# Kernel tuning notes

Hardware: AMD Instinct MI355X
Metric: run time of the kernel (lower is better)

The kernel has to match this reference:

```python
import jax, jax.numpy as jnp
import numpy as np

HID = 128
NEG = 9000000000000000.0  # 9e15 additive mask constant from the source


def setup_inputs() -> dict:
    key = jax.random.key(0)
    ks = jax.random.split(key, 20)
    B, N, OBS, N1, N2 = 32, 2048, 256, 8, 8
    x = jax.random.normal(ks[0], (B, N, OBS), dtype=jnp.float32)
    mask = jax.random.randint(ks[1], (B, N, N), 0, 2).astype(jnp.float32)

    def lin(kw, kb, fan_in, fan_out):
        bound = 1.0 / np.sqrt(fan_in)
        W = jax.random.uniform(kw, (fan_in, fan_out), jnp.float32, -bound, bound)
        b = jax.random.uniform(kb, (fan_out,), jnp.float32, -bound, bound)
        return W, b

    Wv, bv = lin(ks[2], ks[3], OBS, HID)
    Wk, bk = lin(ks[4], ks[5], OBS, HID)
    Wq, bq = lin(ks[6], ks[7], OBS, HID)
    Wout, bout = lin(ks[8], ks[9], HID, HID)
    Wval, bval = lin(ks[10], ks[11], HID, 1)
    Wadv1, badv1 = lin(ks[12], ks[13], HID, N1)
    Wadv2, badv2 = lin(ks[14], ks[15], HID, N2)
    return {
        'x': x, 'mask': mask,
        'Wv': Wv, 'bv': bv, 'Wk': Wk, 'bk': bk, 'Wq': Wq, 'bq': bq,
        'Wout': Wout, 'bout': bout, 'Wval': Wval, 'bval': bval,
        'Wadv1': Wadv1, 'badv1': badv1, 'Wadv2': Wadv2, 'badv2': badv2,
    }


def reference(x, mask, Wv, bv, Wk, bk, Wq, bq, Wout, bout,
              Wval, bval, Wadv1, badv1, Wadv2, badv2):
    # AttenModel
    v = jax.nn.relu(x @ Wv + bv)          # [B,N,H]
    q = jax.nn.relu(x @ Wq + bq)          # [B,N,H]
    k = jax.nn.relu(x @ Wk + bk)          # [B,N,H]
    scores = jnp.einsum('bnh,bmh->bnm', q, k)          # [B,N,N]
    scores = scores * mask - NEG * (1.0 - mask)
    att = jax.nn.softmax(scores, axis=2)
    out = jnp.einsum('bnm,bmh->bnh', att, v)            # [B,N,H]
    out = jax.nn.relu(out @ Wout + bout)                # [B,N,H]
    # Dueling heads (batch > 1, so squeeze(0) is a no-op)
    value = out @ Wval + bval                            # [B,N,1]
    adv1 = out @ Wadv1 + badv1                           # [B,N,n1]
    adv2 = out @ Wadv2 + badv2                           # [B,N,n2]
    q1 = value + adv1 - adv1.mean(axis=1, keepdims=True)
    q2 = value + adv2 - adv2.mean(axis=1, keepdims=True)
    return (q1, q2)
```

## Files before the change

### kernel.cpp

```cpp
#include <hip/hip_runtime.h>
#include <hip/hip_bf16.h>


typedef __attribute__((ext_vector_type(4))) float f32x4;
typedef __attribute__((ext_vector_type(8))) short bf16x8;
typedef __attribute__((ext_vector_type(4))) unsigned int u32x4;

#define LOG2E 1.44269504088896340736f
#define NEGC 9.0e15f

static __device__ __forceinline__ unsigned short f2bf(float f) {
  unsigned int x = __builtin_bit_cast(unsigned int, f);
  unsigned int r = (x + 0x7fffu + ((x >> 16) & 1u)) >> 16;
  return (unsigned short)r;
}
static __device__ __forceinline__ float bf2f(unsigned short u) {
  return __builtin_bit_cast(float, ((unsigned int)u) << 16);
}
static __device__ __forceinline__ unsigned int pack2bf(float lo, float hi) {
  return (unsigned int)f2bf(lo) | ((unsigned int)f2bf(hi) << 16);
}
static __device__ __forceinline__ f32x4 mfma16(bf16x8 a, bf16x8 b, f32x4 c) {
  return __builtin_amdgcn_mfma_f32_16x16x32_bf16(a, b, c, 0, 0, 0);
}

__global__ __launch_bounds__(256) void prepack_kernel(const float* __restrict__ mask,
                                                      unsigned long long* __restrict__ bits) {
  const int lane = threadIdx.x & 63;
  const int gwave = (blockIdx.x << 2) | (threadIdx.x >> 6);
  for (int r = 0; r < 8; ++r) {
    const long row = (long)gwave * 8 + r;
    const float* mp = mask + row * 2048 + lane;
    unsigned long long* op = bits + row * 32;
#pragma unroll
    for (int g = 0; g < 8; ++g) {
      float f0 = mp[(g * 4 + 0) * 64];
      float f1 = mp[(g * 4 + 1) * 64];
      float f2 = mp[(g * 4 + 2) * 64];
      float f3 = mp[(g * 4 + 3) * 64];
      unsigned long long b0 = __ballot(f0 != 0.0f);
      unsigned long long b1 = __ballot(f1 != 0.0f);
      unsigned long long b2 = __ballot(f2 != 0.0f);
      unsigned long long b3 = __ballot(f3 != 0.0f);
      if (lane == 0) {
        ulonglong2 w0 = {b0, b1};
        ulonglong2 w1 = {b2, b3};
        *(ulonglong2*)(op + g * 4) = w0;
        *(ulonglong2*)(op + g * 4 + 2) = w1;
      }
    }
  }
}

__global__ __launch_bounds__(256) void prep_kernel(
    const float* __restrict__ Wv, const float* __restrict__ Wk,
    const float* __restrict__ Wq, const float* __restrict__ Wout,
    unsigned short* __restrict__ Wf_hi, unsigned short* __restrict__ Wf_lo,
    unsigned short* __restrict__ WoutT) {
  int gid = blockIdx.x * 256 + threadIdx.x;
  if (gid < 12288) {
    int kc = gid / 1536;
    int rem = gid - kc * 1536;
    int t = rem >> 6, lane = rem & 63;
    int hf = lane & 15, qf = lane >> 4;
    int sec = t >> 3;
    int j = (t & 7) * 16 + hf;
    const float* W = (sec == 0) ? Wq : (sec == 1) ? Wk : Wv;
#pragma unroll
    for (int e = 0; e < 8; ++e) {
      int k = kc * 32 + qf * 8 + e;
      float w = W[k * 128 + j];
      unsigned short hi = f2bf(w);
      Wf_hi[gid * 8 + e] = hi;
      Wf_lo[gid * 8 + e] = f2bf(w - bf2f(hi));
    }
  } else if (gid < 12288 + 16384) {
    int i2 = gid - 12288;
    int j = i2 >> 7, c = i2 & 127;
    WoutT[i2] = f2bf(Wout[c * 128 + j]);
  }
}

__global__ __launch_bounds__(512, 2) void proj_kernel(
    const float* __restrict__ x,
    const unsigned short* __restrict__ Wf_hi, const unsigned short* __restrict__ Wf_lo,
    const float* __restrict__ bq, const float* __restrict__ bk, const float* __restrict__ bv,
    unsigned short* __restrict__ q_bf, unsigned short* __restrict__ Kf,
    unsigned short* __restrict__ Vf) {
  __shared__ bf16x8 wst_hi[1536];
  __shared__ bf16x8 wst_lo[1536];
  __shared__ unsigned short vbuf[128][136];

  const int tid = threadIdx.x;
  const int lane = tid & 63, wid = tid >> 6;
  const int qq = lane >> 4, hh = lane & 15;
  const long rbase = (long)blockIdx.x * 128;
  const long rowA = rbase + wid * 16 + hh;
  const f32x4 zero4 = {0.f, 0.f, 0.f, 0.f};
  f32x4 acc[24];
#pragma unroll
  for (int t = 0; t < 24; ++t) acc[t] = zero4;

  for (int kc = 0; kc < 8; ++kc) {
    __syncthreads();
#pragma unroll
    for (int i = 0; i < 3; ++i) {
      int idx = i * 512 + tid;
      wst_hi[idx] = *(const bf16x8*)(Wf_hi + ((long)kc * 1536 + idx) * 8);
      wst_lo[idx] = *(const bf16x8*)(Wf_lo + ((long)kc * 1536 + idx) * 8);
    }
    __syncthreads();

    const float* xp = x + rowA * 256 + kc * 32 + qq * 8;
    f32x4 x0 = *(const f32x4*)xp;
    f32x4 x1 = *(const f32x4*)(xp + 4);
    bf16x8 ah, al;
#pragma unroll
    for (int j = 0; j < 8; ++j) {
      float f = (j < 4) ? x0[j] : x1[j - 4];
      unsigned short h = f2bf(f);
      ah[j] = (short)h;
      al[j] = (short)f2bf(f - bf2f(h));
    }
#pragma unroll
    for (int t = 0; t < 24; ++t) {
      bf16x8 bh = wst_hi[t * 64 + lane];
      bf16x8 bl = wst_lo[t * 64 + lane];
      acc[t] = mfma16(ah, bh, acc[t]);
      acc[t] = mfma16(al, bh, acc[t]);
      acc[t] = mfma16(ah, bl, acc[t]);
    }
  }

  const int rowL = wid * 16 + qq * 4;
  const int b = (int)(rbase >> 11);
  const int tbase = (int)((rbase & 2047) >> 6);

  for (int sec = 0; sec < 3; ++sec) {
    __syncthreads();
#pragma unroll
    for (int tp = 0; tp < 8; ++tp) {
      const int t = sec * 8 + tp;
      const int j = tp * 16 + hh;
      const float bias = (sec == 0) ? bq[j] : (sec == 1) ? bk[j] : bv[j];
#pragma unroll
      for (int r = 0; r < 4; ++r) {
        unsigned short h = f2bf(fmaxf(acc[t][r] + bias, 0.f));
        if (sec == 2) vbuf[j][rowL + r] = h;
        else          vbuf[rowL + r][j] = h;
      }
    }
    __syncthreads();
    if (sec == 0) {
      const int row = tid >> 2, ch = tid & 3;
      bf16x8 w = *(const bf16x8*)&vbuf[row][ch * 32];
      bf16x8 w2 = *(const bf16x8*)&vbuf[row][ch * 32 + 8];
      bf16x8 w3 = *(const bf16x8*)&vbuf[row][ch * 32 + 16];
      bf16x8 w4 = *(const bf16x8*)&vbuf[row][ch * 32 + 24];
      unsigned short* op = q_bf + (rbase + row) * 128 + ch * 32;
      *(bf16x8*)op = w; *(bf16x8*)(op + 8) = w2;
      *(bf16x8*)(op + 16) = w3; *(bf16x8*)(op + 24) = w4;
    } else if (sec == 1) {
#pragma unroll
      for (int it = 0; it < 4; ++it) {
        int gid = it * 512 + tid;
        int tt = gid >> 10, m = (gid >> 8) & 3, kc = (gid >> 6) & 3, ln = gid & 63;
        int hf = ln & 15, qf = ln >> 4;
        bf16x8 w = *(const bf16x8*)&vbuf[tt * 64 + m * 16 + hf][kc * 32 + qf * 8];
        long off = (((long)(b * 32 + tbase + tt) * 16 + m * 4 + kc) * 64 + ln) * 8;
        *(bf16x8*)(Kf + off) = w;
      }
    } else {
#pragma unroll
      for (int it = 0; it < 4; ++it) {
        int gid = it * 512 + tid;
        int tt = gid >> 10, ht = (gid >> 7) & 7, c = (gid >> 6) & 1, ln = gid & 63;
        int hf = ln & 15, qf = ln >> 4;
        bf16x8 w = *(const bf16x8*)&vbuf[ht * 16 + hf][tt * 64 + c * 32 + qf * 8];
        long off = (((long)(b * 32 + tbase + tt) * 16 + ht * 2 + c) * 64 + ln) * 8;
        *(bf16x8*)(Vf + off) = w;
      }
    }
  }
}

__global__ __launch_bounds__(512, 2) void attn_kernel(
    const unsigned short* __restrict__ q_bf, const unsigned short* __restrict__ Kf,
    const unsigned short* __restrict__ Vf,
    const unsigned long long* __restrict__ bits, unsigned short* __restrict__ out_att) {
  __shared__ bf16x8 kls[2][1024];
  __shared__ bf16x8 vls[2][1024];

  const int tid = threadIdx.x;
  const int lane = tid & 63, wid = tid >> 6;
  const int qq = lane >> 4, hh = lane & 15;
  const int orig = blockIdx.x;
  const int b = ((orig & 7) << 2) | ((orig >> 3) & 3);
  const int nb = orig >> 5;
  const long qbase = (long)b * 2048 + nb * 256 + wid * 32;

  const f32x4 zero4 = {0.f, 0.f, 0.f, 0.f};

  bf16x8 qh[2][4];
#pragma unroll
  for (int ctq = 0; ctq < 2; ++ctq)
#pragma unroll
    for (int kc = 0; kc < 4; ++kc)
      qh[ctq][kc] = *(const bf16x8*)(q_bf + (qbase + ctq * 16 + hh) * 128 + kc * 32 + qq * 8);

  const unsigned long long* br0 = bits + (qbase + hh) * 32;
  const unsigned long long* br1 = bits + (qbase + 16 + hh) * 32;
  const unsigned short* kf0 = Kf + (long)(b * 32) * 8192;
  const unsigned short* vf0 = Vf + (long)(b * 32) * 8192;

  f32x4 o_acc[8][2];
#pragma unroll
  for (int ht = 0; ht < 8; ++ht) { o_acc[ht][0] = zero4; o_acc[ht][1] = zero4; }
  float m_run[2] = {-3.0e38f, -3.0e38f};
  float l_run[2] = {0.f, 0.f};

  bf16x8 stg[4];
  const int seg0 = wid * 4;
  auto LOADREG = [&](int t) {
#pragma unroll
    for (int i = 0; i < 4; ++i) {
      int seg = seg0 + i;
      const unsigned short* src = (seg < 16)
          ? kf0 + (long)t * 8192 + (seg * 64 + lane) * 8
          : vf0 + (long)t * 8192 + ((seg - 16) * 64 + lane) * 8;
      stg[i] = *(const bf16x8*)src;
    }
  };
  auto WRITEBUF = [&](int nb2) {
#pragma unroll
    for (int i = 0; i < 4; ++i) {
      int seg = seg0 + i;
      if (seg < 16) kls[nb2][seg * 64 + lane] = stg[i];
      else          vls[nb2][(seg - 16) * 64 + lane] = stg[i];
    }
  };

  LOADREG(0);
  WRITEBUF(0);
  LOADREG(1);
  __syncthreads();

  unsigned long long bc0 = br0[0];
  unsigned long long bc1 = br1[0];

  const int src0 = (((qq << 1)) & 3) * 16 + hh;
  const int src1 = (((qq << 1) + 1) & 3) * 16 + hh;
  const bool hiq = qq >= 2;
  int cur = 0;

  for (int t = 0; t < 32; ++t) {
    unsigned long long bn0 = 0, bn1 = 0;
    if (t + 1 < 32) { bn0 = br0[t + 1]; bn1 = br1[t + 1]; }

    f32x4 s[2][4];
#pragma unroll
    for (int m = 0; m < 4; ++m) { s[0][m] = zero4; s[1][m] = zero4; }
#pragma unroll
    for (int m = 0; m < 4; ++m) {
      bf16x8 khf[4];
#pragma unroll
      for (int kc = 0; kc < 4; ++kc) khf[kc] = kls[cur][(m * 4 + kc) * 64 + lane];
#pragma unroll
      for (int kc = 0; kc < 4; ++kc)
#pragma unroll
        for (int ctq = 0; ctq < 2; ++ctq)
          s[ctq][m] = mfma16(khf[kc], qh[ctq][kc], s[ctq][m]);
    }

    {
      const unsigned long long bb0 = bc0 >> (qq * 4);
      const unsigned long long bb1 = bc1 >> (qq * 4);
#pragma unroll
      for (int m = 0; m < 4; ++m)
#pragma unroll
        for (int r = 0; r < 4; ++r) {
          const int sh = m * 16 + r;
          s[0][m][r] = ((bb0 >> sh) & 1ull) ? s[0][m][r] : -NEGC;
          s[1][m][r] = ((bb1 >> sh) & 1ull) ? s[1][m][r] : -NEGC;
        }
    }

    unsigned int pk[2][4][2];
#pragma unroll
    for (int ctq = 0; ctq < 2; ++ctq) {
      float mx = s[ctq][0][0];
#pragma unroll
      for (int m = 0; m < 4; ++m)
#pragma unroll
        for (int r = 0; r < 4; ++r) mx = fmaxf(mx, s[ctq][m][r]);
      mx = fmaxf(mx, __shfl_xor(mx, 16, 64));
      mx = fmaxf(mx, __shfl_xor(mx, 32, 64));
      if (__any(mx > m_run[ctq])) {
        float mnew = fmaxf(m_run[ctq], mx);
        float sc = exp2f((m_run[ctq] - mnew) * LOG2E);
        m_run[ctq] = mnew;
        l_run[ctq] *= sc;
#pragma unroll
        for (int ht = 0; ht < 8; ++ht) o_acc[ht][ctq] *= sc;
      }
      float ps = 0.f;
#pragma unroll
      for (int m = 0; m < 4; ++m)
#pragma unroll
        for (int r = 0; r < 4; ++r) {
          float p = exp2f((s[ctq][m][r] - m_run[ctq]) * LOG2E);
          s[ctq][m][r] = p;
          ps += p;
        }
      ps += __shfl_xor(ps, 16, 64);
      ps += __shfl_xor(ps, 32, 64);
      l_run[ctq] += ps;
#pragma unroll
      for (int m = 0; m < 4; ++m) {
        pk[ctq][m][0] = pack2bf(s[ctq][m][0], s[ctq][m][1]);
        pk[ctq][m][1] = pack2bf(s[ctq][m][2], s[ctq][m][3]);
      }
    }

    bf16x8 pb[2][2];
#pragma unroll
    for (int ctq = 0; ctq < 2; ++ctq)
#pragma unroll
      for (int c = 0; c < 2; ++c) {
        unsigned int a0 = (unsigned int)__shfl((int)pk[ctq][2 * c][0], src0, 64);
        unsigned int a1 = (unsigned int)__shfl((int)pk[ctq][2 * c][1], src0, 64);
        unsigned int a2 = (unsigned int)__shfl((int)pk[ctq][2 * c][0], src1, 64);
        unsigned int a3 = (unsigned int)__shfl((int)pk[ctq][2 * c][1], src1, 64);
        unsigned int b0 = (unsigned int)__shfl((int)pk[ctq][2 * c + 1][0], src0, 64);
        unsigned int b1 = (unsigned int)__shfl((int)pk[ctq][2 * c + 1][1], src0, 64);
        unsigned int b2 = (unsigned int)__shfl((int)pk[ctq][2 * c + 1][0], src1, 64);
        unsigned int b3 = (unsigned int)__shfl((int)pk[ctq][2 * c + 1][1], src1, 64);
        u32x4 w;
        w[0] = hiq ? b0 : a0;
        w[1] = hiq ? b1 : a1;
        w[2] = hiq ? b2 : a2;
        w[3] = hiq ? b3 : a3;
        pb[ctq][c] = __builtin_bit_cast(bf16x8, w);
      }

#pragma unroll
    for (int ht = 0; ht < 8; ++ht)
#pragma unroll
      for (int c = 0; c < 2; ++c) {
        bf16x8 vf = vls[cur][(ht * 2 + c) * 64 + lane];
#pragma unroll
        for (int ctq = 0; ctq < 2; ++ctq)
          o_acc[ht][ctq] = mfma16(vf, pb[ctq][c], o_acc[ht][ctq]);
      }

    __syncthreads();
    if (t + 1 < 32) WRITEBUF(cur ^ 1);
    if (t + 2 < 32) LOADREG(t + 2);
    __syncthreads();
    cur ^= 1;
    bc0 = bn0;
    bc1 = bn1;
  }

#pragma unroll
  for (int ctq = 0; ctq < 2; ++ctq) {
    float inv = 1.0f / l_run[ctq];
    const long row = qbase + ctq * 16 + hh;
#pragma unroll
    for (int ht = 0; ht < 8; ++ht) {
      f32x4 o = o_acc[ht][ctq];
      uint2 w;
      w.x = pack2bf(o[0] * inv, o[1] * inv);
      w.y = pack2bf(o[2] * inv, o[3] * inv);
      *(uint2*)(out_att + row * 128 + ht * 16 + qq * 4) = w;
    }
  }
}

__global__ __launch_bounds__(256) void wout_heads_kernel(
    const unsigned short* __restrict__ out_att, const unsigned short* __restrict__ WoutT,
    const float* __restrict__ bout,
    const float* __restrict__ Wval, const float* __restrict__ bval,
    const float* __restrict__ Wadv1, const float* __restrict__ badv1,
    const float* __restrict__ Wadv2, const float* __restrict__ badv2,
    float* __restrict__ value, float* __restrict__ adv1, float* __restrict__ adv2) {
  const int lane = threadIdx.x & 63, wid = threadIdx.x >> 6;
  const int qq = lane >> 4, hh = lane & 15;
  const long rowA = (long)blockIdx.x * 64 + wid * 16 + hh;
  const f32x4 zero4 = {0.f, 0.f, 0.f, 0.f};
  f32x4 acc[8];
#pragma unroll
  for (int t = 0; t < 8; ++t) acc[t] = zero4;
#pragma unroll
  for (int kc = 0; kc < 4; ++kc) {
    bf16x8 af = *(const bf16x8*)(out_att + rowA * 128 + kc * 32 + qq * 8);
#pragma unroll
    for (int t = 0; t < 8; ++t) {
      bf16x8 bf = *(const bf16x8*)(WoutT + (t * 16 + hh) * 128 + kc * 32 + qq * 8);
      acc[t] = mfma16(af, bf, acc[t]);
    }
  }
  float pv[4] = {0.f, 0.f, 0.f, 0.f};
  float pa1[4][8], pa2[4][8];
#pragma unroll
  for (int r = 0; r < 4; ++r)
#pragma unroll
    for (int j = 0; j < 8; ++j) { pa1[r][j] = 0.f; pa2[r][j] = 0.f; }
#pragma unroll
  for (int t = 0; t < 8; ++t) {
    const int col = t * 16 + hh;
    const float bo = bout[col];
    const float wv = Wval[col];
    const f32x4 w1a = *(const f32x4*)(Wadv1 + col * 8);
    const f32x4 w1b = *(const f32x4*)(Wadv1 + col * 8 + 4);
    const f32x4 w2a = *(const f32x4*)(Wadv2 + col * 8);
    const f32x4 w2b = *(const f32x4*)(Wadv2 + col * 8 + 4);
#pragma unroll
    for (int r = 0; r < 4; ++r) {
      float h = fmaxf(acc[t][r] + bo, 0.f);
      pv[r] += h * wv;
#pragma unroll
      for (int j = 0; j < 4; ++j) {
        pa1[r][j]     += h * w1a[j];
        pa1[r][4 + j] += h * w1b[j];
        pa2[r][j]     += h * w2a[j];
        pa2[r][4 + j] += h * w2b[j];
      }
    }
  }
#pragma unroll
  for (int r = 0; r < 4; ++r) {
#pragma unroll
    for (int s = 1; s < 16; s <<= 1) {
      pv[r] += __shfl_xor(pv[r], s, 64);
#pragma unroll
      for (int j = 0; j < 8; ++j) {
        pa1[r][j] += __shfl_xor(pa1[r][j], s, 64);
        pa2[r][j] += __shfl_xor(pa2[r][j], s, 64);
      }
    }
  }
  if (hh == 0) {
    const float bv0 = bval[0];
#pragma unroll
    for (int r = 0; r < 4; ++r) {
      const long row = (long)blockIdx.x * 64 + wid * 16 + qq * 4 + r;
      value[row] = pv[r] + bv0;
#pragma unroll
      for (int j = 0; j < 8; ++j) {
        adv1[row * 8 + j] = pa1[r][j] + badv1[j];
        adv2[row * 8 + j] = pa2[r][j] + badv2[j];
      }
    }
  }
}

__global__ __launch_bounds__(256) void sums_kernel(const float* __restrict__ adv1,
                                                   const float* __restrict__ adv2,
                                                   float* __restrict__ sums) {
  const int b = blockIdx.x, tid = threadIdx.x;
  __shared__ float red[4][16];
  float p[16];
#pragma unroll
  for (int j = 0; j < 16; ++j) p[j] = 0.f;
  for (int n = tid; n < 2048; n += 256) {
    const long row = (long)b * 2048 + n;
    const f32x4 a1a = *(const f32x4*)(adv1 + row * 8);
    const f32x4 a1b = *(const f32x4*)(adv1 + row * 8 + 4);
    const f32x4 a2a = *(const f32x4*)(adv2 + row * 8);
    const f32x4 a2b = *(const f32x4*)(adv2 + row * 8 + 4);
#pragma unroll
    for (int j = 0; j < 4; ++j) {
      p[j] += a1a[j]; p[4 + j] += a1b[j];
      p[8 + j] += a2a[j]; p[12 + j] += a2b[j];
    }
  }
#pragma unroll
  for (int s = 1; s < 64; s <<= 1)
#pragma unroll
    for (int j = 0; j < 16; ++j) p[j] += __shfl_xor(p[j], s, 64);
  const int wid = tid >> 6;
  if ((tid & 63) == 0)
#pragma unroll
    for (int j = 0; j < 16; ++j) red[wid][j] = p[j];
  __syncthreads();
  if (tid < 16)
    sums[b * 16 + tid] = red[0][tid] + red[1][tid] + red[2][tid] + red[3][tid];
}

__global__ void combine_kernel(const float* __restrict__ value, const float* __restrict__ adv1,
                               const float* __restrict__ adv2, const float* __restrict__ sums,
                               float* __restrict__ out) {
  const int idx = blockIdx.x * 256 + threadIdx.x;
  const int half = 524288;
  const int which = (idx >= half) ? 1 : 0;
  const int rem = idx - which * half;
  const int b = rem >> 14;
  const int r2 = rem & 16383;
  const int n = r2 >> 3, j = r2 & 7;
  const long row = (long)b * 2048 + n;
  const float* adv = which ? adv2 : adv1;
  const float mean = sums[b * 16 + which * 8 + j] * (1.0f / 2048.0f);
  out[idx] = value[row] + adv[row * 8 + j] - mean;
}

extern "C" void kernel_launch(void* const* d_in, const int* in_sizes, int n_in,
                              void* d_out, int out_size, void* d_ws, size_t ws_size,
                              hipStream_t stream) {
  const float* x     = (const float*)d_in[0];
  const float* mask  = (const float*)d_in[1];
  const float* Wv    = (const float*)d_in[2];
  const float* bv    = (const float*)d_in[3];
  const float* Wk    = (const float*)d_in[4];
  const float* bk    = (const float*)d_in[5];
  const float* Wq    = (const float*)d_in[6];
  const float* bq    = (const float*)d_in[7];
  const float* Wout  = (const float*)d_in[8];
  const float* bout  = (const float*)d_in[9];
  const float* Wval  = (const float*)d_in[10];
  const float* bval  = (const float*)d_in[11];
  const float* Wadv1 = (const float*)d_in[12];
  const float* badv1 = (const float*)d_in[13];
  const float* Wadv2 = (const float*)d_in[14];
  const float* badv2 = (const float*)d_in[15];
  float* out = (float*)d_out;
  char* ws = (char*)d_ws;

  unsigned short* q_bf   = (unsigned short*)(ws + 0);
  unsigned short* Kf     = (unsigned short*)(ws + 16777216);
  unsigned short* Vf     = (unsigned short*)(ws + 33554432);
  unsigned short* out_at = (unsigned short*)(ws + 50331648);
  float* value = (float*)(ws + 67108864);
  float* adv1  = (float*)(ws + 67371008);
  float* adv2  = (float*)(ws + 69468160);
  float* sums  = (float*)(ws + 71565312);
  unsigned short* Wf_hi = (unsigned short*)(ws + 71567360);
  unsigned short* Wf_lo = (unsigned short*)(ws + 71763968);
  unsigned short* WoutT = (unsigned short*)(ws + 71960576);
  unsigned long long* bits = (unsigned long long*)(ws + 71993344);

  prepack_kernel<<<2048, 256, 0, stream>>>(mask, bits);
  prep_kernel<<<112, 256, 0, stream>>>(Wv, Wk, Wq, Wout, Wf_hi, Wf_lo, WoutT);
  proj_kernel<<<512, 512, 0, stream>>>(x, Wf_hi, Wf_lo, bq, bk, bv, q_bf, Kf, Vf);
  attn_kernel<<<256, 512, 0, stream>>>(q_bf, Kf, Vf, bits, out_at);
  wout_heads_kernel<<<1024, 256, 0, stream>>>(out_at, WoutT, bout, Wval, bval,
                                              Wadv1, badv1, Wadv2, badv2,
                                              value, adv1, adv2);
  sums_kernel<<<32, 256, 0, stream>>>(adv1, adv2, sums);
  combine_kernel<<<4096, 256, 0, stream>>>(value, adv1, adv2, sums, out);
}
```

Baseline: 362.9 us.

## Overlap LDS buffer writes with MFMA compute, vectorize mask bit-packing

The attention loop now writes the next K/V tile into the alternate LDS buffer and issues the following global load at the start of each iteration, before the MFMA work. This drops one of the two barriers per iteration and lets stores overlap with compute. MFMA sections are wrapped in s_setprio to favour matrix issue across waves. The mask prepack kernel switches from per-element ballots to float4 loads plus nibble packing combined with xor shuffles, giving coalesced vector reads.

```diff
diff --git a/kernel.cpp b/kernel.cpp
--- a/kernel.cpp
+++ b/kernel.cpp
@@ -28,26 +28,22 @@
                                                       unsigned long long* __restrict__ bits) {
   const int lane = threadIdx.x & 63;
   const int gwave = (blockIdx.x << 2) | (threadIdx.x >> 6);
+  const int sub = lane & 15, grp = lane >> 4;
   for (int r = 0; r < 8; ++r) {
     const long row = (long)gwave * 8 + r;
-    const float* mp = mask + row * 2048 + lane;
+    const float* mp = mask + row * 2048;
     unsigned long long* op = bits + row * 32;
 #pragma unroll
     for (int g = 0; g < 8; ++g) {
-      float f0 = mp[(g * 4 + 0) * 64];
-      float f1 = mp[(g * 4 + 1) * 64];
-      float f2 = mp[(g * 4 + 2) * 64];
-      float f3 = mp[(g * 4 + 3) * 64];
-      unsigned long long b0 = __ballot(f0 != 0.0f);
-      unsigned long long b1 = __ballot(f1 != 0.0f);
-      unsigned long long b2 = __ballot(f2 != 0.0f);
-      unsigned long long b3 = __ballot(f3 != 0.0f);
-      if (lane == 0) {
-        ulonglong2 w0 = {b0, b1};
-        ulonglong2 w1 = {b2, b3};
-        *(ulonglong2*)(op + g * 4) = w0;
-        *(ulonglong2*)(op + g * 4 + 2) = w1;
-      }
+      f32x4 v = *(const f32x4*)(mp + g * 256 + lane * 4);
+      unsigned int nib = (v[0] != 0.f ? 1u : 0u) | (v[1] != 0.f ? 2u : 0u)
+                       | (v[2] != 0.f ? 4u : 0u) | (v[3] != 0.f ? 8u : 0u);
+      unsigned long long val = (unsigned long long)nib << (sub * 4);
+      val |= __shfl_xor(val, 1, 64);
+      val |= __shfl_xor(val, 2, 64);
+      val |= __shfl_xor(val, 4, 64);
+      val |= __shfl_xor(val, 8, 64);
+      if (sub == 0) op[g * 4 + grp] = val;
     }
   }
 }
@@ -257,9 +253,13 @@
     unsigned long long bn0 = 0, bn1 = 0;
     if (t + 1 < 32) { bn0 = br0[t + 1]; bn1 = br1[t + 1]; }
 
+    if (t + 1 < 32) WRITEBUF(cur ^ 1);
+    if (t + 2 < 32) LOADREG(t + 2);
+
     f32x4 s[2][4];
 #pragma unroll
     for (int m = 0; m < 4; ++m) { s[0][m] = zero4; s[1][m] = zero4; }
+    __builtin_amdgcn_s_setprio(1);
 #pragma unroll
     for (int m = 0; m < 4; ++m) {
       bf16x8 khf[4];
@@ -271,6 +271,7 @@
         for (int ctq = 0; ctq < 2; ++ctq)
           s[ctq][m] = mfma16(khf[kc], qh[ctq][kc], s[ctq][m]);
     }
+    __builtin_amdgcn_s_setprio(0);
 
     {
       const unsigned long long bb0 = bc0 >> (qq * 4);
@@ -343,6 +344,7 @@
         pb[ctq][c] = __builtin_bit_cast(bf16x8, w);
       }
 
+    __builtin_amdgcn_s_setprio(1);
 #pragma unroll
     for (int ht = 0; ht < 8; ++ht)
 #pragma unroll
@@ -352,10 +354,8 @@
         for (int ctq = 0; ctq < 2; ++ctq)
           o_acc[ht][ctq] = mfma16(vf, pb[ctq][c], o_acc[ht][ctq]);
       }
-
-    __syncthreads();
-    if (t + 1 < 32) WRITEBUF(cur ^ 1);
-    if (t + 2 < 32) LOADREG(t + 2);
+    __builtin_amdgcn_s_setprio(0);
+
     __syncthreads();
     cur ^= 1;
     bc0 = bn0;
```

Result: no change. 359.5 us (-0.9%).
